# Optimization experiments

Hardware: AMD Instinct MI355X
Metric: run time of the kernel (lower is better)

Reference implementation:

```python
import jax, jax.numpy as jnp
import numpy as np

B = 2097152  # batch
H = 9        # hidden width
N_MID = 19   # fc2..fc20


def setup_inputs() -> dict:
    key = jax.random.key(0)
    ks = jax.random.split(key, 8)
    x = jax.random.normal(ks[0], (B, 2), dtype=jnp.float32)
    # PyTorch Linear init: U(-1/sqrt(fan_in), 1/sqrt(fan_in))
    def lin(k, out_f, in_f):
        kw, kb = jax.random.split(k)
        bound = 1.0 / np.sqrt(in_f)
        W = jax.random.uniform(kw, (out_f, in_f), jnp.float32, -bound, bound)
        b = jax.random.uniform(kb, (out_f,), jnp.float32, -bound, bound)
        return W, b
    W1, b1 = lin(ks[1], H, 2)
    # stacked middle layers fc2..fc20: [19, 9, 9] / [19, 9]
    kmids = jax.random.split(ks[2], N_MID)
    Wmid = jnp.stack([lin(k, H, H)[0] for k in kmids])
    bmid = jnp.stack([lin(jax.random.fold_in(k, 1), H, H)[1] for k in kmids])
    W21, b21 = lin(ks[3], 2, H)
    return {"x": x, "W1": W1, "b1": b1, "Wmid": Wmid, "bmid": bmid,
            "W21": W21, "b21": b21}


def reference(x, W1, b1, Wmid, bmid, W21, b21):
    h = jax.nn.elu(x @ W1.T + b1)  # [B, 9]
    def layer(h, wb):
        W, b = wb
        return jax.nn.elu(h @ W.T + b), None
    h, _ = jax.lax.scan(layer, h, (Wmid, bmid))
    logits = h @ W21.T + b21  # [B, 2]
    return jax.nn.log_softmax(logits, axis=1)
```

## Files before the change

### kernel.cpp

```cpp
#include <hip/hip_runtime.h>


typedef _Float16 half8 __attribute__((ext_vector_type(8)));
typedef _Float16 h2 __attribute__((ext_vector_type(2)));
typedef float float4v __attribute__((ext_vector_type(4)));
typedef unsigned int uint4v __attribute__((ext_vector_type(4)));

extern "C" __device__ _Float16 __ocml_exp2_f16(_Float16);

constexpr int H   = 9;
constexpr int NL  = 21;
constexpr int TPW = 16;
constexpr int NCH = 4;
constexpr int NPS = TPW / NCH;
constexpr int BLK = 64;

__global__ void build_frags(const float* __restrict__ W1, const float* __restrict__ b1,
                            const float* __restrict__ Wmid, const float* __restrict__ bmid,
                            const float* __restrict__ W21, const float* __restrict__ b21,
                            _Float16* __restrict__ ws) {
    const float L   = 1.4426950408889634f;
    const float LN2 = 0.6931471805599453f;
    int l    = blockIdx.x;
    int lane = threadIdx.x;
    int row  = lane & 15;
    int g    = lane >> 4;
    bool orow = ((row & 3) != 3) && (row < 12);
    int  o    = row - (row >> 2);
    for (int j = 0; j < 8; ++j) {
        int k = g * 8 + j;
        float v = 0.0f;
        if (l == 0) {
            if (orow && k < 2)        v = L * W1[o * 2 + k];
            else if (orow && k == 27) v = L * b1[o];
        } else if (l <= 19) {
            const float* W = Wmid + (l - 1) * 81;
            const float* b = bmid + (l - 1) * 9;
            if (orow) {
                if (j < 3 && g < 3) {
                    int r_in = g * 4 + j;
                    int i = r_in - (r_in >> 2);
                    v = W[o * 9 + i];
                } else if (j >= 4 && j < 7 && g < 3) {
                    int r_in = g * 4 + (j - 4);
                    int i = r_in - (r_in >> 2);
                    v = L * W[o * 9 + i];
                } else if (k == 27) {
                    float s = 0.0f;
                    for (int i = 0; i < H; ++i) s += W[o * 9 + i];
                    v = L * (b[o] - s);
                }
            }
        } else {
            if (row < 2) {
                if (j < 3 && g < 3) {
                    int r_in = g * 4 + j;
                    int i = r_in - (r_in >> 2);
                    v = LN2 * W21[row * 9 + i];
                } else if (j >= 4 && j < 7 && g < 3) {
                    int r_in = g * 4 + (j - 4);
                    int i = r_in - (r_in >> 2);
                    v = W21[row * 9 + i];
                } else if (k == 27) {
                    float s = 0.0f;
                    for (int i = 0; i < H; ++i) s += W21[row * 9 + i];
                    v = b21[row] - s;
                }
            }
        }
        ws[l * 512 + lane * 8 + j] = (_Float16)v;
    }
}

__device__ __forceinline__ half8 act_to_b(float4v d) {
    const h2 Z = {(_Float16)0.f, (_Float16)0.f};
    h2 p01 = __builtin_bit_cast(h2, __builtin_amdgcn_cvt_pkrtz(d[0], d[1]));
    h2 p2b = __builtin_bit_cast(h2, __builtin_amdgcn_cvt_pkrtz(d[2], 1.0f));
    h2 r01 = __builtin_elementwise_max(p01, Z);
    h2 r2b = __builtin_elementwise_max(p2b, Z);
    h2 t01 = __builtin_elementwise_min(p01, Z);
    h2 t2b = __builtin_elementwise_min(p2b, Z);
    h2 e01 = __builtin_elementwise_exp2(t01);
    _Float16 e2 = __ocml_exp2_f16(t2b[0]);
    uint4v u;
    u[0] = __builtin_bit_cast(unsigned, r01);
    u[1] = __builtin_bit_cast(unsigned, r2b);
    u[2] = __builtin_bit_cast(unsigned, e01);
    u[3] = 0x3C000000u |
           (unsigned)__builtin_bit_cast(unsigned short, e2);
    return __builtin_bit_cast(half8, u);
}

__device__ __forceinline__ float bperm(int byte_idx, float v) {
    return __builtin_bit_cast(float,
        __builtin_amdgcn_ds_bpermute(byte_idx, __builtin_bit_cast(int, v)));
}

__device__ __forceinline__ void softmax4(const float4v* dd, int gbase,
                                         int lane, int grp,
                                         float* __restrict__ out) {
    const float NLOG2E = -1.4426950408889634f;
    const float LN2f   = 0.6931471805599453f;
    const int bidx = (lane & 15) << 2;
    float a0 = bperm(bidx, dd[0][0]), a1 = bperm(bidx, dd[0][1]);
    float b0 = bperm(bidx, dd[1][0]), b1 = bperm(bidx, dd[1][1]);
    float c0 = bperm(bidx, dd[2][0]), c1 = bperm(bidx, dd[2][1]);
    float d0 = bperm(bidx, dd[3][0]), d1 = bperm(bidx, dd[3][1]);
    float l0 = (grp == 0) ? a0 : (grp == 1) ? b0 : (grp == 2) ? c0 : d0;
    float l1 = (grp == 0) ? a1 : (grp == 1) ? b1 : (grp == 2) ? c1 : d1;
    float mx  = fmaxf(l0, l1);
    float ad  = fabsf(l0 - l1);
    float e   = __builtin_amdgcn_exp2f(NLOG2E * ad);
    float lg  = __builtin_amdgcn_logf(1.0f + e);
    float lse = fmaf(LN2f, lg, mx);
    ((float2*)out)[(gbase << 4) + lane] = make_float2(l0 - lse, l1 - lse);
}

__global__ __launch_bounds__(BLK, 4) void mlp_mfma(const float* __restrict__ x,
                                                   const _Float16* __restrict__ ws,
                                                   float* __restrict__ out) {
    const int lane  = threadIdx.x;
    const int grp   = lane >> 4;
    const int col   = lane & 15;
    const int tile0 = blockIdx.x * TPW;

    const half8* wsv = (const half8*)ws;
    const unsigned g0_sel  = (grp == 0) ? 0xFFFFFFFFu : 0u;
    const unsigned bias_u1 = (grp == 3) ? 0x3C000000u : 0u;
    const float4v ZV = {0.f, 0.f, 0.f, 0.f};

    unsigned xb[TPW];
    #pragma unroll
    for (int k = 0; k < TPW; ++k) {
        float2 xv = ((const float2*)x)[((tile0 + k) << 4) + col];
        xb[k] = __builtin_bit_cast(unsigned,
                    __builtin_amdgcn_cvt_pkrtz(xv.x, xv.y)) & g0_sel;
    }

    #pragma unroll
    for (int pass = 0; pass < NPS; ++pass) {
        half8 bf[NCH];
        #pragma unroll
        for (int k = 0; k < NCH; ++k) {
            uint4v u;
            u[0] = xb[pass * NCH + k];
            u[1] = bias_u1;
            u[2] = 0u; u[3] = 0u;
            bf[k] = __builtin_bit_cast(half8, u);
        }

        float4v dd[NCH];
        #pragma unroll
        for (int l = 0; l < NL; ++l) {
            half8 A = wsv[l * 64 + lane];
            #pragma unroll
            for (int k = 0; k < NCH; ++k)
                dd[k] = __builtin_amdgcn_mfma_f32_16x16x32_f16(A, bf[k], ZV, 0, 0, 0);
            if (l < NL - 1) {
                #pragma unroll
                for (int k = 0; k < NCH; ++k)
                    bf[k] = act_to_b(dd[k]);
            }
        }

        softmax4(dd, tile0 + pass * NCH, lane, grp, out);
    }
}

extern "C" void kernel_launch(void* const* d_in, const int* in_sizes, int n_in,
                              void* d_out, int out_size, void* d_ws, size_t ws_size,
                              hipStream_t stream) {
    const float* x    = (const float*)d_in[0];
    const float* W1   = (const float*)d_in[1];
    const float* b1   = (const float*)d_in[2];
    const float* Wmid = (const float*)d_in[3];
    const float* bmid = (const float*)d_in[4];
    const float* W21  = (const float*)d_in[5];
    const float* b21  = (const float*)d_in[6];
    float* out = (float*)d_out;
    _Float16* ws = (_Float16*)d_ws;

    build_frags<<<NL, 64, 0, stream>>>(W1, b1, Wmid, bmid, W21, b21, ws);

    const int nrows = in_sizes[0] / 2;
    const int tiles = nrows / 16;
    const int blocks = tiles / TPW;
    mlp_mfma<<<blocks, BLK, 0, stream>>>(x, ws, out);
}
```

Baseline: 154.5 us.

## Fold ELU split into single activation term and use 16x16x16 MFMA

The ELU is now computed as one combined value (relu scaled by ln2 plus exp2 of the negative part) per hidden unit, rather than feeding relu and exp parts as separate K entries. This halves the K dimension, so the weight fragments shrink to half4 and the MFMA becomes 16x16x16 instead of 16x16x32, which halves weight loads and cuts packing work. The third activation element is computed in fp32 with an extra FMA. Folding the -1 into the bias and mixing precisions may shift numerical accuracy slightly.

```diff
diff --git a/kernel.cpp b/kernel.cpp
--- a/kernel.cpp
+++ b/kernel.cpp
@@ -1,12 +1,10 @@
 #include <hip/hip_runtime.h>
 
 
-typedef _Float16 half8 __attribute__((ext_vector_type(8)));
+typedef _Float16 half4v __attribute__((ext_vector_type(4)));
 typedef _Float16 h2 __attribute__((ext_vector_type(2)));
 typedef float float4v __attribute__((ext_vector_type(4)));
-typedef unsigned int uint4v __attribute__((ext_vector_type(4)));
-
-extern "C" __device__ _Float16 __ocml_exp2_f16(_Float16);
+typedef unsigned int uint2v __attribute__((ext_vector_type(2)));
 
 constexpr int H   = 9;
 constexpr int NL  = 21;
@@ -19,76 +17,62 @@
                             const float* __restrict__ Wmid, const float* __restrict__ bmid,
                             const float* __restrict__ W21, const float* __restrict__ b21,
                             _Float16* __restrict__ ws) {
-    const float L   = 1.4426950408889634f;
-    const float LN2 = 0.6931471805599453f;
+    const float L = 1.4426950408889634f;
     int l    = blockIdx.x;
     int lane = threadIdx.x;
     int row  = lane & 15;
     int g    = lane >> 4;
     bool orow = ((row & 3) != 3) && (row < 12);
     int  o    = row - (row >> 2);
-    for (int j = 0; j < 8; ++j) {
-        int k = g * 8 + j;
+    for (int j = 0; j < 4; ++j) {
+        int k = g * 4 + j;
+        bool kreal = ((k & 3) < 3) && (k < 12);
+        int  i     = k - (k >> 2);
         float v = 0.0f;
         if (l == 0) {
             if (orow && k < 2)        v = L * W1[o * 2 + k];
-            else if (orow && k == 27) v = L * b1[o];
+            else if (orow && k == 15) v = L * b1[o];
         } else if (l <= 19) {
             const float* W = Wmid + (l - 1) * 81;
             const float* b = bmid + (l - 1) * 9;
             if (orow) {
-                if (j < 3 && g < 3) {
-                    int r_in = g * 4 + j;
-                    int i = r_in - (r_in >> 2);
-                    v = W[o * 9 + i];
-                } else if (j >= 4 && j < 7 && g < 3) {
-                    int r_in = g * 4 + (j - 4);
-                    int i = r_in - (r_in >> 2);
+                if (kreal) {
                     v = L * W[o * 9 + i];
-                } else if (k == 27) {
+                } else if (k == 15) {
                     float s = 0.0f;
-                    for (int i = 0; i < H; ++i) s += W[o * 9 + i];
+                    for (int t = 0; t < H; ++t) s += W[o * 9 + t];
                     v = L * (b[o] - s);
                 }
             }
         } else {
             if (row < 2) {
-                if (j < 3 && g < 3) {
-                    int r_in = g * 4 + j;
-                    int i = r_in - (r_in >> 2);
-                    v = LN2 * W21[row * 9 + i];
-                } else if (j >= 4 && j < 7 && g < 3) {
-                    int r_in = g * 4 + (j - 4);
-                    int i = r_in - (r_in >> 2);
+                if (kreal) {
                     v = W21[row * 9 + i];
-                } else if (k == 27) {
+                } else if (k == 15) {
                     float s = 0.0f;
-                    for (int i = 0; i < H; ++i) s += W21[row * 9 + i];
+                    for (int t = 0; t < H; ++t) s += W21[row * 9 + t];
                     v = b21[row] - s;
                 }
             }
         }
-        ws[l * 512 + lane * 8 + j] = (_Float16)v;
+        ws[l * 256 + lane * 4 + j] = (_Float16)v;
     }
 }
 
-__device__ __forceinline__ half8 act_to_b(float4v d) {
-    const h2 Z = {(_Float16)0.f, (_Float16)0.f};
+__device__ __forceinline__ void act(float4v d, unsigned &w0, unsigned &w1) {
+    const h2 Z    = {(_Float16)0.f, (_Float16)0.f};
+    const h2 LN2H = {(_Float16)0.6931471805599453f, (_Float16)0.6931471805599453f};
     h2 p01 = __builtin_bit_cast(h2, __builtin_amdgcn_cvt_pkrtz(d[0], d[1]));
-    h2 p2b = __builtin_bit_cast(h2, __builtin_amdgcn_cvt_pkrtz(d[2], 1.0f));
     h2 r01 = __builtin_elementwise_max(p01, Z);
-    h2 r2b = __builtin_elementwise_max(p2b, Z);
     h2 t01 = __builtin_elementwise_min(p01, Z);
-    h2 t2b = __builtin_elementwise_min(p2b, Z);
     h2 e01 = __builtin_elementwise_exp2(t01);
-    _Float16 e2 = __ocml_exp2_f16(t2b[0]);
-    uint4v u;
-    u[0] = __builtin_bit_cast(unsigned, r01);
-    u[1] = __builtin_bit_cast(unsigned, r2b);
-    u[2] = __builtin_bit_cast(unsigned, e01);
-    u[3] = 0x3C000000u |
-           (unsigned)__builtin_bit_cast(unsigned short, e2);
-    return __builtin_bit_cast(half8, u);
+    h2 s01 = __builtin_elementwise_fma(r01, LN2H, e01);
+    w0 = __builtin_bit_cast(unsigned, s01);
+    float r2 = fmaxf(d[2], 0.0f);
+    float t2 = fminf(d[2], 0.0f);
+    float e2 = __builtin_amdgcn_exp2f(t2);
+    float s2 = fmaf(r2, 0.6931471805599453f, e2);
+    w1 = __builtin_bit_cast(unsigned, __builtin_amdgcn_cvt_pkrtz(s2, 1.0f));
 }
 
 __device__ __forceinline__ float bperm(int byte_idx, float v) {
@@ -124,8 +108,7 @@
     const int col   = lane & 15;
     const int tile0 = blockIdx.x * TPW;
 
-    const half8* wsv = (const half8*)ws;
-    const unsigned g0_sel  = (grp == 0) ? 0xFFFFFFFFu : 0u;
+    const half4v* wsv = (const half4v*)ws;
     const unsigned bias_u1 = (grp == 3) ? 0x3C000000u : 0u;
     const float4v ZV = {0.f, 0.f, 0.f, 0.f};
 
@@ -134,32 +117,32 @@
     for (int k = 0; k < TPW; ++k) {
         float2 xv = ((const float2*)x)[((tile0 + k) << 4) + col];
         xb[k] = __builtin_bit_cast(unsigned,
-                    __builtin_amdgcn_cvt_pkrtz(xv.x, xv.y)) & g0_sel;
+                    __builtin_amdgcn_cvt_pkrtz(xv.x, xv.y));
     }
 
     #pragma unroll
     for (int pass = 0; pass < NPS; ++pass) {
-        half8 bf[NCH];
+        unsigned w0[NCH], w1[NCH];
         #pragma unroll
         for (int k = 0; k < NCH; ++k) {
-            uint4v u;
-            u[0] = xb[pass * NCH + k];
-            u[1] = bias_u1;
-            u[2] = 0u; u[3] = 0u;
-            bf[k] = __builtin_bit_cast(half8, u);
+            w0[k] = xb[pass * NCH + k];
+            w1[k] = bias_u1;
         }
 
         float4v dd[NCH];
         #pragma unroll
         for (int l = 0; l < NL; ++l) {
-            half8 A = wsv[l * 64 + lane];
+            half4v A = wsv[l * 64 + lane];
             #pragma unroll
-            for (int k = 0; k < NCH; ++k)
-                dd[k] = __builtin_amdgcn_mfma_f32_16x16x32_f16(A, bf[k], ZV, 0, 0, 0);
+            for (int k = 0; k < NCH; ++k) {
+                uint2v u = {w0[k], w1[k]};
+                dd[k] = __builtin_amdgcn_mfma_f32_16x16x16f16(
+                            A, __builtin_bit_cast(half4v, u), ZV, 0, 0, 0);
+            }
             if (l < NL - 1) {
                 #pragma unroll
                 for (int k = 0; k < NCH; ++k)
-                    bf[k] = act_to_b(dd[k]);
+                    act(dd[k], w0[k], w1[k]);
             }
         }
 
```

Measured after the change: 158.5 us. +2.6%, slower.
